# Kernel optimization log

Hardware: AMD Instinct MI355X
Metric: run time of the kernel (lower is better)

Reference implementation:

```python
import jax, jax.numpy as jnp
import numpy as np

INPUT_DIM = 2048
N_EXPERTS = 64
K = 2


def setup_inputs() -> dict:
    key = jax.random.key(0)
    kx, kw, kb = jax.random.split(key, 3)
    x = jax.random.normal(kx, (4, 4096, INPUT_DIM), dtype=jnp.float32)
    # nn.Linear(input_dim, n_experts): weight [n_experts, input_dim], bias [n_experts]
    bound = 1.0 / np.sqrt(INPUT_DIM)
    W = jax.random.uniform(kw, (N_EXPERTS, INPUT_DIM), minval=-bound, maxval=bound, dtype=jnp.float32)
    b = jax.random.uniform(kb, (N_EXPERTS,), minval=-bound, maxval=bound, dtype=jnp.float32)
    return {"x": x, "W": W, "b": b}


def reference(x, W, b):
    # logits: [B, S, E]
    logits = jnp.einsum('bsd,ed->bse', x, W) + b
    topk_vals, topk_indices = jax.lax.top_k(logits, K)  # over last (expert) axis
    gate_probs = jax.nn.softmax(topk_vals, axis=-1)
    return gate_probs, topk_indices
```

## Files before the change

### kernel.cpp

```cpp
#include <hip/hip_runtime.h>
#include <math.h>
#include <stdint.h>

typedef _Float16 half8 __attribute__((ext_vector_type(8)));
typedef float floatx4 __attribute__((ext_vector_type(4)));

#define NTOK   16384
#define DIM    2048
#define NEXP   64
#define TPB    16
#define NBLK   (NTOK / TPB)
#define NCHW   8
#define WSW_H8 16384
#define WSW_BYTES (2 * WSW_H8 * 16)

#define ABUF_BYTES 32768
#define RED_STRIDE 68
#define RED_F      (4 * 16 * RED_STRIDE)

__global__ void wprep_kernel(const float* __restrict__ W, _Float16* __restrict__ wsw) {
    const int id   = blockIdx.x * blockDim.x + threadIdx.x;
    const int lane = id & 63;
    const int tg   = (id >> 6) & 3;
    const int sg   = id >> 8;
    const int e    = tg * 16 + (lane & 15);
    const int k    = sg * 32 + (lane >> 4) * 8;
    const float* src = W + (size_t)e * DIM + k;
    half8 h, l;
#pragma unroll
    for (int j = 0; j < 8; j++) {
        const float v  = src[j];
        const _Float16 hh = (_Float16)v;
        h[j] = hh;
        l[j] = (_Float16)((v - (float)hh) * 2048.0f);
    }
    const size_t slot = (size_t)(sg * 4 + tg) * 64 + lane;
    ((half8*)wsw)[slot]          = h;
    ((half8*)wsw)[WSW_H8 + slot] = l;
}

__device__ __forceinline__ void split_a(const float4& v0, const float4& v1,
                                        half8& hi, half8& lo) {
    const float av[8] = {v0.x, v0.y, v0.z, v0.w, v1.x, v1.y, v1.z, v1.w};
#pragma unroll
    for (int j = 0; j < 8; j++) {
        const _Float16 hh = (_Float16)av[j];
        hi[j] = hh;
        lo[j] = (_Float16)((av[j] - (float)hh) * 2048.0f);
    }
}

__device__ __forceinline__ void dma16(const void* g, const char* l) {
    __builtin_amdgcn_global_load_lds(
        (const __attribute__((address_space(1))) unsigned int*)(uintptr_t)g,
        (__attribute__((address_space(3))) unsigned int*)(uintptr_t)l,
        16, 0, 0);
}

template <bool USE_WS> struct BFrag;
template <> struct BFrag<true>  { half8  h[2][4]; half8 l[2][4]; };
template <> struct BFrag<false> { float4 a[2][4][2]; };

template <bool USE_WS>
__device__ __forceinline__ void load_b(BFrag<USE_WS>& bf, const half8* wb,
                                       const float* Wb, int cc) {
    if constexpr (USE_WS) {
#pragma unroll
        for (int s = 0; s < 2; s++)
#pragma unroll
            for (int t = 0; t < 4; t++) {
                const size_t o = (size_t)(cc * 8 + s * 4 + t) * 64;
                bf.h[s][t] = wb[o];
                bf.l[s][t] = wb[o + WSW_H8];
            }
    } else {
#pragma unroll
        for (int s = 0; s < 2; s++)
#pragma unroll
            for (int t = 0; t < 4; t++) {
                const float* wr = Wb + (size_t)(t * 16) * DIM + cc * 64 + s * 32;
                bf.a[s][t][0] = *(const float4*)wr;
                bf.a[s][t][1] = *(const float4*)(wr + 4);
            }
    }
}

template <bool USE_WS>
__global__ __launch_bounds__(256, 3)
void gating_kernel(const float* __restrict__ x, const float* __restrict__ W,
                   const _Float16* __restrict__ wsw, const float* __restrict__ bias,
                   float* __restrict__ out)
{
    __shared__ char  abuf[ABUF_BYTES];
    __shared__ float red[RED_F];

    const int tid  = threadIdx.x;
    const int lane = tid & 63;
    const int ks   = tid >> 6;
    const int col  = lane & 15;
    const int quad = lane >> 4;
    const int tok0 = blockIdx.x * TPB;

    const float* gA[4];
#pragma unroll
    for (int i = 0; i < 4; i++) {
        const int row = i * 4 + quad;
        const int pz  = col;
        const int gp  = (pz & 8) | ((pz & 7) ^ (row & 7));
        gA[i] = x + (size_t)(tok0 + row) * DIM + ks * (NCHW * 64) + gp * 4;
    }
    char* const ab = abuf + ks * 8192;
    const half8* wb = (const half8*)wsw + (size_t)ks * 4096 + lane;
    const float* Wb = W + (size_t)col * DIM + ks * (NCHW * 64) + quad * 8;

    floatx4 accm[4] = {{0,0,0,0},{0,0,0,0},{0,0,0,0},{0,0,0,0}};
    floatx4 accl[4] = {{0,0,0,0},{0,0,0,0},{0,0,0,0},{0,0,0,0}};

#pragma unroll
    for (int i = 0; i < 4; i++) dma16(gA[i], ab + i * 1024);
    asm volatile("" ::: "memory");
    BFrag<USE_WS> bc;
    load_b<USE_WS>(bc, wb, Wb, 0);
#pragma unroll
    for (int i = 0; i < 4; i++) dma16(gA[i] + 64, ab + 4096 + i * 1024);

#pragma unroll
    for (int cc = 0; cc < NCHW; ++cc) {
        if (cc == NCHW - 1) asm volatile("s_waitcnt vmcnt(16)" ::: "memory");
        else                asm volatile("s_waitcnt vmcnt(20)" ::: "memory");
        const char* Ab = ab + (cc & 1) * 4096;
        float4 v0[2], v1[2];
#pragma unroll
        for (int s = 0; s < 2; s++) {
            v0[s] = *(const float4*)(Ab + col * 256 + (8 * s + ((2 * quad + 0) ^ (col & 7))) * 16);
            v1[s] = *(const float4*)(Ab + col * 256 + (8 * s + ((2 * quad + 1) ^ (col & 7))) * 16);
        }
        asm volatile("s_waitcnt lgkmcnt(0)" ::: "memory");
        BFrag<USE_WS> bn;
        if (cc + 1 < NCHW) load_b<USE_WS>(bn, wb, Wb, cc + 1);
        if (cc + 2 < NCHW) {
#pragma unroll
            for (int i = 0; i < 4; i++)
                dma16(gA[i] + (size_t)(cc + 2) * 64, ab + (cc & 1) * 4096 + i * 1024);
        }
#pragma unroll
        for (int s = 0; s < 2; s++) {
            half8 ah, al;
            split_a(v0[s], v1[s], ah, al);
#pragma unroll
            for (int t = 0; t < 4; t++) {
                half8 bh, bl;
                if constexpr (USE_WS) {
                    bh = bc.h[s][t];
                    bl = bc.l[s][t];
                } else {
                    split_a(bc.a[s][t][0], bc.a[s][t][1], bh, bl);
                }
                accm[t] = __builtin_amdgcn_mfma_f32_16x16x32_f16(ah, bh, accm[t], 0, 0, 0);
                accl[t] = __builtin_amdgcn_mfma_f32_16x16x32_f16(ah, bl, accl[t], 0, 0, 0);
                accl[t] = __builtin_amdgcn_mfma_f32_16x16x32_f16(al, bh, accl[t], 0, 0, 0);
            }
        }
        if (cc + 1 < NCHW) bc = bn;
    }

    const float inv = 1.0f / 2048.0f;
#pragma unroll
    for (int t = 0; t < 4; t++)
#pragma unroll
        for (int r = 0; r < 4; r++)
            red[(ks * 16 + quad * 4 + r) * RED_STRIDE + t * 16 + col] =
                accm[t][r] + accl[t][r] * inv;
    __syncthreads();

    if (tid < TPB) {
        const int tk = tid;
        float v0 = -INFINITY, v1 = -INFINITY;
        int   i0 = 0, i1 = 0;
        for (int e = 0; e < NEXP; e++) {
            const float v = red[(0 * 16 + tk) * RED_STRIDE + e]
                          + red[(1 * 16 + tk) * RED_STRIDE + e]
                          + red[(2 * 16 + tk) * RED_STRIDE + e]
                          + red[(3 * 16 + tk) * RED_STRIDE + e] + bias[e];
            if (v > v0)      { v1 = v0; i1 = i0; v0 = v; i0 = e; }
            else if (v > v1) { v1 = v; i1 = e; }
        }
        const float e1 = expf(v1 - v0);
        const float sden = 1.f + e1;
        const int   g  = tok0 + tk;
        out[2 * g + 0] = 1.f / sden;
        out[2 * g + 1] = e1 / sden;
        out[2 * NTOK + 2 * g + 0] = (float)i0;
        out[2 * NTOK + 2 * g + 1] = (float)i1;
    }
}

extern "C" void kernel_launch(void* const* d_in, const int* in_sizes, int n_in,
                              void* d_out, int out_size, void* d_ws, size_t ws_size,
                              hipStream_t stream) {
    const float* x    = (const float*)d_in[0];
    const float* W    = (const float*)d_in[1];
    const float* bias = (const float*)d_in[2];
    float*       out  = (float*)d_out;
    _Float16*    wsw  = (_Float16*)d_ws;

    if (ws_size >= (size_t)WSW_BYTES) {
        hipLaunchKernelGGL(wprep_kernel, dim3(64), dim3(256), 0, stream, W, wsw);
        hipLaunchKernelGGL((gating_kernel<true>), dim3(NBLK), dim3(256), 0, stream,
                           x, W, wsw, bias, out);
    } else {
        hipLaunchKernelGGL((gating_kernel<false>), dim3(NBLK), dim3(256), 0, stream,
                           x, W, wsw, bias, out);
    }
}
```

Before: 211.1 us.

## Rewrite gating GEMM with 32-token blocks, register pipelining, on-the-fly W split

Drops the W pre-split kernel and the LDS DMA staging of x. Each block now handles 32 tokens, with two 16-row M tiles per wave reusing the same W fragments, so W traffic per token is halved. x and W are loaded straight into registers with a triple-buffered (x) and double-buffered (W) prefetch. W is split into hi/lo fp16 inside the kernel for every block, and bias is staged in shared memory. The cost is extra split arithmetic, more register pressure (occupancy hint lowered to 2), and uncoalesced direct global loads with no LDS swizzle.

```diff
diff --git a/kernel.cpp b/kernel.cpp
--- a/kernel.cpp
+++ b/kernel.cpp
@@ -5,42 +5,19 @@
 typedef _Float16 half8 __attribute__((ext_vector_type(8)));
 typedef float floatx4 __attribute__((ext_vector_type(4)));
 
-#define NTOK   16384
-#define DIM    2048
-#define NEXP   64
-#define TPB    16
-#define NBLK   (NTOK / TPB)
-#define NCHW   8
-#define WSW_H8 16384
-#define WSW_BYTES (2 * WSW_H8 * 16)
+#define NTOK 16384
+#define DIM  2048
+#define NEXP 64
+#define TPB  32
+#define NBLK (NTOK / TPB)
+#define KSPL 4
+#define KW   (DIM / KSPL)
+#define NST  (KW / 32)
+#define RSTR 68
+#define REDF (KSPL * TPB * RSTR)
 
-#define ABUF_BYTES 32768
-#define RED_STRIDE 68
-#define RED_F      (4 * 16 * RED_STRIDE)
-
-__global__ void wprep_kernel(const float* __restrict__ W, _Float16* __restrict__ wsw) {
-    const int id   = blockIdx.x * blockDim.x + threadIdx.x;
-    const int lane = id & 63;
-    const int tg   = (id >> 6) & 3;
-    const int sg   = id >> 8;
-    const int e    = tg * 16 + (lane & 15);
-    const int k    = sg * 32 + (lane >> 4) * 8;
-    const float* src = W + (size_t)e * DIM + k;
-    half8 h, l;
-#pragma unroll
-    for (int j = 0; j < 8; j++) {
-        const float v  = src[j];
-        const _Float16 hh = (_Float16)v;
-        h[j] = hh;
-        l[j] = (_Float16)((v - (float)hh) * 2048.0f);
-    }
-    const size_t slot = (size_t)(sg * 4 + tg) * 64 + lane;
-    ((half8*)wsw)[slot]          = h;
-    ((half8*)wsw)[WSW_H8 + slot] = l;
-}
-
-__device__ __forceinline__ void split_a(const float4& v0, const float4& v1,
-                                        half8& hi, half8& lo) {
+__device__ __forceinline__ void split8(const float4& v0, const float4& v1,
+                                       half8& hi, half8& lo) {
     const float av[8] = {v0.x, v0.y, v0.z, v0.w, v1.x, v1.y, v1.z, v1.w};
 #pragma unroll
     for (int j = 0; j < 8; j++) {
@@ -50,49 +27,12 @@
     }
 }
 
-__device__ __forceinline__ void dma16(const void* g, const char* l) {
-    __builtin_amdgcn_global_load_lds(
-        (const __attribute__((address_space(1))) unsigned int*)(uintptr_t)g,
-        (__attribute__((address_space(3))) unsigned int*)(uintptr_t)l,
-        16, 0, 0);
-}
-
-template <bool USE_WS> struct BFrag;
-template <> struct BFrag<true>  { half8  h[2][4]; half8 l[2][4]; };
-template <> struct BFrag<false> { float4 a[2][4][2]; };
-
-template <bool USE_WS>
-__device__ __forceinline__ void load_b(BFrag<USE_WS>& bf, const half8* wb,
-                                       const float* Wb, int cc) {
-    if constexpr (USE_WS) {
-#pragma unroll
-        for (int s = 0; s < 2; s++)
-#pragma unroll
-            for (int t = 0; t < 4; t++) {
-                const size_t o = (size_t)(cc * 8 + s * 4 + t) * 64;
-                bf.h[s][t] = wb[o];
-                bf.l[s][t] = wb[o + WSW_H8];
-            }
-    } else {
-#pragma unroll
-        for (int s = 0; s < 2; s++)
-#pragma unroll
-            for (int t = 0; t < 4; t++) {
-                const float* wr = Wb + (size_t)(t * 16) * DIM + cc * 64 + s * 32;
-                bf.a[s][t][0] = *(const float4*)wr;
-                bf.a[s][t][1] = *(const float4*)(wr + 4);
-            }
-    }
-}
-
-template <bool USE_WS>
-__global__ __launch_bounds__(256, 3)
+__global__ __launch_bounds__(256, 2)
 void gating_kernel(const float* __restrict__ x, const float* __restrict__ W,
-                   const _Float16* __restrict__ wsw, const float* __restrict__ bias,
-                   float* __restrict__ out)
+                   const float* __restrict__ bias, float* __restrict__ out)
 {
-    __shared__ char  abuf[ABUF_BYTES];
-    __shared__ float red[RED_F];
+    __shared__ float red[REDF];
+    __shared__ float bsh[NEXP];
 
     const int tid  = threadIdx.x;
     const int lane = tid & 63;
@@ -100,77 +40,83 @@
     const int col  = lane & 15;
     const int quad = lane >> 4;
     const int tok0 = blockIdx.x * TPB;
+    const int k0   = ks * KW;
 
-    const float* gA[4];
+    if (tid < NEXP) bsh[tid] = bias[tid];
+
+    const float* pA[2];
 #pragma unroll
-    for (int i = 0; i < 4; i++) {
-        const int row = i * 4 + quad;
-        const int pz  = col;
-        const int gp  = (pz & 8) | ((pz & 7) ^ (row & 7));
-        gA[i] = x + (size_t)(tok0 + row) * DIM + ks * (NCHW * 64) + gp * 4;
-    }
-    char* const ab = abuf + ks * 8192;
-    const half8* wb = (const half8*)wsw + (size_t)ks * 4096 + lane;
-    const float* Wb = W + (size_t)col * DIM + ks * (NCHW * 64) + quad * 8;
+    for (int m = 0; m < 2; m++)
+        pA[m] = x + (size_t)(tok0 + m * 16 + col) * DIM + k0 + quad * 8;
+    const float* pB[4];
+#pragma unroll
+    for (int t = 0; t < 4; t++)
+        pB[t] = W + (size_t)(t * 16 + col) * DIM + k0 + quad * 8;
 
-    floatx4 accm[4] = {{0,0,0,0},{0,0,0,0},{0,0,0,0},{0,0,0,0}};
-    floatx4 accl[4] = {{0,0,0,0},{0,0,0,0},{0,0,0,0},{0,0,0,0}};
+    float4 Ab[3][2][2];
+    float4 Bb[2][4][2];
+    floatx4 accm[2][4];
+    floatx4 accl[2][4];
+#pragma unroll
+    for (int m = 0; m < 2; m++)
+#pragma unroll
+        for (int t = 0; t < 4; t++) { accm[m][t] = (floatx4){0,0,0,0}; accl[m][t] = (floatx4){0,0,0,0}; }
 
 #pragma unroll
-    for (int i = 0; i < 4; i++) dma16(gA[i], ab + i * 1024);
-    asm volatile("" ::: "memory");
-    BFrag<USE_WS> bc;
-    load_b<USE_WS>(bc, wb, Wb, 0);
+    for (int s = 0; s < 2; s++)
 #pragma unroll
-    for (int i = 0; i < 4; i++) dma16(gA[i] + 64, ab + 4096 + i * 1024);
+        for (int m = 0; m < 2; m++)
+#pragma unroll
+            for (int h = 0; h < 2; h++)
+                Ab[s][m][h] = *(const float4*)(pA[m] + s * 32 + h * 4);
+#pragma unroll
+    for (int t = 0; t < 4; t++)
+#pragma unroll
+        for (int h = 0; h < 2; h++)
+            Bb[0][t][h] = *(const float4*)(pB[t] + h * 4);
 
 #pragma unroll
-    for (int cc = 0; cc < NCHW; ++cc) {
-        if (cc == NCHW - 1) asm volatile("s_waitcnt vmcnt(16)" ::: "memory");
-        else                asm volatile("s_waitcnt vmcnt(20)" ::: "memory");
-        const char* Ab = ab + (cc & 1) * 4096;
-        float4 v0[2], v1[2];
+    for (int s = 0; s < NST; s++) {
+        if (s + 2 < NST) {
 #pragma unroll
-        for (int s = 0; s < 2; s++) {
-            v0[s] = *(const float4*)(Ab + col * 256 + (8 * s + ((2 * quad + 0) ^ (col & 7))) * 16);
-            v1[s] = *(const float4*)(Ab + col * 256 + (8 * s + ((2 * quad + 1) ^ (col & 7))) * 16);
+            for (int m = 0; m < 2; m++)
+#pragma unroll
+                for (int h = 0; h < 2; h++)
+                    Ab[(s + 2) % 3][m][h] = *(const float4*)(pA[m] + (s + 2) * 32 + h * 4);
         }
-        asm volatile("s_waitcnt lgkmcnt(0)" ::: "memory");
-        BFrag<USE_WS> bn;
-        if (cc + 1 < NCHW) load_b<USE_WS>(bn, wb, Wb, cc + 1);
-        if (cc + 2 < NCHW) {
+        if (s + 1 < NST) {
 #pragma unroll
-            for (int i = 0; i < 4; i++)
-                dma16(gA[i] + (size_t)(cc + 2) * 64, ab + (cc & 1) * 4096 + i * 1024);
+            for (int t = 0; t < 4; t++)
+#pragma unroll
+                for (int h = 0; h < 2; h++)
+                    Bb[(s + 1) & 1][t][h] = *(const float4*)(pB[t] + (s + 1) * 32 + h * 4);
         }
+        half8 ah[2], al[2];
 #pragma unroll
-        for (int s = 0; s < 2; s++) {
-            half8 ah, al;
-            split_a(v0[s], v1[s], ah, al);
+        for (int m = 0; m < 2; m++)
+            split8(Ab[s % 3][m][0], Ab[s % 3][m][1], ah[m], al[m]);
 #pragma unroll
-            for (int t = 0; t < 4; t++) {
-                half8 bh, bl;
-                if constexpr (USE_WS) {
-                    bh = bc.h[s][t];
-                    bl = bc.l[s][t];
-                } else {
-                    split_a(bc.a[s][t][0], bc.a[s][t][1], bh, bl);
-                }
-                accm[t] = __builtin_amdgcn_mfma_f32_16x16x32_f16(ah, bh, accm[t], 0, 0, 0);
-                accl[t] = __builtin_amdgcn_mfma_f32_16x16x32_f16(ah, bl, accl[t], 0, 0, 0);
-                accl[t] = __builtin_amdgcn_mfma_f32_16x16x32_f16(al, bh, accl[t], 0, 0, 0);
+        for (int t = 0; t < 4; t++) {
+            half8 bh, bl;
+            split8(Bb[s & 1][t][0], Bb[s & 1][t][1], bh, bl);
+#pragma unroll
+            for (int m = 0; m < 2; m++) {
+                accm[m][t] = __builtin_amdgcn_mfma_f32_16x16x32_f16(ah[m], bh, accm[m][t], 0, 0, 0);
+                accl[m][t] = __builtin_amdgcn_mfma_f32_16x16x32_f16(ah[m], bl, accl[m][t], 0, 0, 0);
+                accl[m][t] = __builtin_amdgcn_mfma_f32_16x16x32_f16(al[m], bh, accl[m][t], 0, 0, 0);
             }
         }
-        if (cc + 1 < NCHW) bc = bn;
     }
 
     const float inv = 1.0f / 2048.0f;
 #pragma unroll
     for (int t = 0; t < 4; t++)
 #pragma unroll
-        for (int r = 0; r < 4; r++)
-            red[(ks * 16 + quad * 4 + r) * RED_STRIDE + t * 16 + col] =
-                accm[t][r] + accl[t][r] * inv;
+        for (int m = 0; m < 2; m++)
+#pragma unroll
+            for (int r = 0; r < 4; r++)
+                red[(ks * TPB + m * 16 + quad * 4 + r) * RSTR + t * 16 + col] =
+                    accm[m][t][r] + accl[m][t][r] * inv;
     __syncthreads();
 
     if (tid < TPB) {
@@ -178,10 +124,10 @@
         float v0 = -INFINITY, v1 = -INFINITY;
         int   i0 = 0, i1 = 0;
         for (int e = 0; e < NEXP; e++) {
-            const float v = red[(0 * 16 + tk) * RED_STRIDE + e]
-                          + red[(1 * 16 + tk) * RED_STRIDE + e]
-                          + red[(2 * 16 + tk) * RED_STRIDE + e]
-                          + red[(3 * 16 + tk) * RED_STRIDE + e] + bias[e];
+            const float v = red[(0 * TPB + tk) * RSTR + e]
+                          + red[(1 * TPB + tk) * RSTR + e]
+                          + red[(2 * TPB + tk) * RSTR + e]
+                          + red[(3 * TPB + tk) * RSTR + e] + bsh[e];
             if (v > v0)      { v1 = v0; i1 = i0; v0 = v; i0 = e; }
             else if (v > v1) { v1 = v; i1 = e; }
         }
@@ -198,18 +144,11 @@
 extern "C" void kernel_launch(void* const* d_in, const int* in_sizes, int n_in,
                               void* d_out, int out_size, void* d_ws, size_t ws_size,
                               hipStream_t stream) {
+    (void)d_ws; (void)ws_size;
     const float* x    = (const float*)d_in[0];
     const float* W    = (const float*)d_in[1];
     const float* bias = (const float*)d_in[2];
     float*       out  = (float*)d_out;
-    _Float16*    wsw  = (_Float16*)d_ws;
-
-    if (ws_size >= (size_t)WSW_BYTES) {
-        hipLaunchKernelGGL(wprep_kernel, dim3(64), dim3(256), 0, stream, W, wsw);
-        hipLaunchKernelGGL((gating_kernel<true>), dim3(NBLK), dim3(256), 0, stream,
-                           x, W, wsw, bias, out);
-    } else {
-        hipLaunchKernelGGL((gating_kernel<false>), dim3(NBLK), dim3(256), 0, stream,
-                           x, W, wsw, bias, out);
-    }
+    hipLaunchKernelGGL(gating_kernel, dim3(NBLK), dim3(256), 0, stream,
+                       x, W, bias, out);
 }
```

Result: slower. 226.1 us (+7.1%).
